# Optimization experiments

Measured on AMD Instinct MI355X. Metric: run time of the kernel, lower is better.

## Reference

```python
import jax, jax.numpy as jnp
import numpy as np

EPS = 1e-5


def _binary_act(x):
    # Forward: sign(x). Backward: piecewise-polynomial surrogate (ApproxSign STE).
    out3 = jnp.where(x < -1, -1.0,
            jnp.where(x < 0, x * x + 2.0 * x,
             jnp.where(x < 1, -x * x + 2.0 * x, 1.0)))
    return jax.lax.stop_gradient(jnp.sign(x) - out3) + out3


def _binarize_weights(w):
    # Per-output-channel scaling factor (detached), forward = scale*sign(w),
    # backward flows through clamp(w, -1, 1) (STE).
    scale = jax.lax.stop_gradient(jnp.mean(jnp.abs(w), axis=(1, 2, 3), keepdims=True))
    clipped = jnp.clip(w, -1.0, 1.0)
    return jax.lax.stop_gradient(scale * jnp.sign(w) - clipped) + clipped


def setup_inputs() -> dict:
    key = jax.random.key(0)
    kx, kw = jax.random.split(key)
    B, Cin, Cout, H, W = 32, 128, 128, 56, 56
    x = jax.random.normal(kx, (B, Cin, H, W), dtype=jnp.float32)
    # HardBinaryConv: weight = rand(n)*0.001 permuted then reshaped -> just random in [0, 0.001)
    w = jax.random.uniform(kw, (Cout, Cin, 3, 3), dtype=jnp.float32) * 0.001
    return {
        "x": x,
        "bias0": jnp.zeros((Cin,), jnp.float32),   # move0 LearnableBias
        "w": w,                                     # HardBinaryConv latent weights
        "gamma": jnp.ones((Cout,), jnp.float32),    # BN weight
        "beta": jnp.zeros((Cout,), jnp.float32),    # BN bias
        "bias1": jnp.zeros((Cout,), jnp.float32),   # move1
        "alpha": jnp.full((Cout,), 0.25, jnp.float32),  # PReLU per-channel
        "bias2": jnp.zeros((Cout,), jnp.float32),   # move2
    }


def reference(x, bias0, w, gamma, beta, bias1, alpha, bias2):
    def pc(v):  # per-channel broadcast (1, C, 1, 1)
        return v[None, :, None, None]

    residual = x
    out = x + pc(bias0)                     # move0
    out = _binary_act(out)                  # binary activation
    bw = _binarize_weights(w)               # {-scale, +scale} weights
    y = jax.lax.conv_general_dilated(
        out, bw, window_strides=(1, 1), padding=((1, 1), (1, 1)),
        dimension_numbers=("NCHW", "OIHW", "NCHW"))
    # BatchNorm2d (training mode: biased batch statistics over N,H,W)
    mean = jnp.mean(y, axis=(0, 2, 3), keepdims=True)
    var = jnp.mean(jnp.square(y - mean), axis=(0, 2, 3), keepdims=True)
    y = (y - mean) * jax.lax.rsqrt(var + EPS) * pc(gamma) + pc(beta)
    y = y + residual
    y = y + pc(bias1)                       # move1
    y = jnp.where(y >= 0, y, pc(alpha) * y)  # PReLU
    y = y + pc(bias2)                       # move2
    return y
```

## Files before the change

### kernel.cpp

```cpp
#include <hip/hip_runtime.h>
#include <stdint.h>

#define NB 32
#define NC 128
#define NH 56
#define NW 56
#define NHW_ (NH * NW)
#define NPIX (NB * NHW_)
#define NO 128
#define NK 1152
#define NSTRIP 14
#define NSLOT (NB * NSTRIP)

#define PADH 58
#define PADW 66
#define PAD_BYTES ((size_t)NB * PADH * PADW * 2 * 8)

typedef unsigned long long u64;

__device__ __forceinline__ size_t pidx(int n, int h, int w) {
    return (((size_t)n * PADH + (h + 1)) * PADW + (w + 1)) * 2;
}

__global__ __launch_bounds__(256) void pack_act(const float* __restrict__ x,
                                                const float* __restrict__ bias0,
                                                u64* __restrict__ packAp) {
    int p = blockIdx.x * 256 + threadIdx.x;
    if (p >= NPIX) return;
    int n = p / NHW_;
    int rem = p - n * NHW_;
    int h = rem / NW, wcol = rem - h * NW;
    const float* xb = x + (size_t)n * NC * NHW_ + rem;
    u64 w0 = 0, w1 = 0;
#pragma unroll 8
    for (int c = 0; c < 64; ++c)
        w0 |= (u64)((xb[(size_t)c * NHW_] + bias0[c]) > 0.f) << c;
#pragma unroll 8
    for (int c = 0; c < 64; ++c)
        w1 |= (u64)((xb[(size_t)(c + 64) * NHW_] + bias0[c + 64]) > 0.f) << c;
    size_t idx = pidx(n, h, wcol);
    packAp[idx]     = w0;
    packAp[idx + 1] = w1;
}

__global__ __launch_bounds__(64) void pack_wgt(const float* __restrict__ w,
                                               u64* __restrict__ packW,
                                               float* __restrict__ scaleW,
                                               int* __restrict__ corrW) {
    __shared__ u64 sb[18];
    int o = blockIdx.x;
    int t = threadIdx.x;
    const float* wo = w + (size_t)o * NK;
    float s = 0.f;
    for (int i = t; i < NK; i += 64) s += fabsf(wo[i]);
    for (int off = 32; off; off >>= 1) s += __shfl_down(s, off);
    if (t == 0) scaleW[o] = s / (float)NK;
    if (t < 18) {
        int tap = t >> 1;
        int j   = t & 1;
        u64 bits = 0;
        for (int cc = 0; cc < 64; ++cc) {
            int c = j * 64 + cc;
            bits |= (u64)(wo[c * 9 + tap] > 0.f) << cc;
        }
        packW[(size_t)o * 18 + t] = bits;
        sb[t] = bits;
    }
    __syncthreads();
    if (t == 0) {
        int cv[9];
#pragma unroll
        for (int tap = 0; tap < 9; ++tap)
            cv[tap] = NC - 2 * (__popcll(sb[2 * tap]) + __popcll(sb[2 * tap + 1]));
        int* cw = corrW + o * 8;
        cw[0] = cv[0] + cv[3] + cv[6];
        cw[1] = cv[2] + cv[5] + cv[8];
        cw[2] = cv[0] + cv[1] + cv[2];
        cw[3] = cv[6] + cv[7] + cv[8];
        cw[4] = cv[0];
        cw[5] = cv[2];
        cw[6] = cv[6];
        cw[7] = cv[8];
    }
}

template <int MODE>
__global__ __launch_bounds__(128, 4) void conv_bin(
    const u64* __restrict__ packAp, const u64* __restrict__ packW,
    const int* __restrict__ corrW, short* __restrict__ yI,
    int* __restrict__ sumP, int* __restrict__ sqP,
    const float* __restrict__ coefA, const float* __restrict__ coefB,
    const float* __restrict__ alpha, const float* __restrict__ bias2,
    const float* __restrict__ x, float* __restrict__ out) {
    __shared__ u64 lw[32 * 18];
    __shared__ int lc[32 * 8];

    int bid = blockIdx.x;
    int n = bid / (NSTRIP * 4);
    int rem = bid - n * (NSTRIP * 4);
    int strip = rem >> 2;
    int cgp = rem & 3;
    int obase = cgp * 32;
    int h0 = strip * 4;

    for (int i = threadIdx.x; i < 32 * 18; i += 128) lw[i] = packW[(size_t)obase * 18 + i];
    for (int i = threadIdx.x; i < 32 * 8; i += 128) lc[i] = corrW[obase * 8 + i];

    int wv = threadIdx.x >> 6, lane = threadIdx.x & 63;
    bool act = lane < NW;

    u64 a[6][3][2];
    const u64* bp = packAp + (((size_t)n * PADH + h0) * PADW + lane) * 2;
#pragma unroll
    for (int r = 0; r < 6; ++r)
#pragma unroll
        for (int c = 0; c < 3; ++c) {
            ulonglong2 q = *reinterpret_cast<const ulonglong2*>(bp + ((size_t)r * PADW + c) * 2);
            a[r][c][0] = q.x;
            a[r][c][1] = q.y;
        }
#pragma unroll
    for (int r = 0; r < 6; ++r)
#pragma unroll
        for (int c = 0; c < 3; ++c)
            asm volatile("" : "+v"(a[r][c][0]), "+v"(a[r][c][1]));
    __syncthreads();

    bool top = (strip == 0), bot = (strip == NSTRIP - 1);
    bool isL = (lane == 0), isR = (lane == NW - 1);
    int sl = n * NSTRIP + strip;
    short* ybase = yI + (size_t)n * NO * NHW_ + (size_t)h0 * NW + lane;

    for (int oo = 0; oo < 16; ++oo) {
        int lo = (wv << 4) + oo;
        int o = obase + lo;
        const u64* wp = &lw[lo * 18];
        int pc0 = 0, pc1 = 0, pc2 = 0, pc3 = 0;
#pragma unroll
        for (int t = 0; t < 9; ++t) {
            const int kh = t / 3, kw = t - 3 * (t / 3);
            u64 w0 = wp[2 * t], w1 = wp[2 * t + 1];
            pc0 += __popcll(a[kh][kw][0] ^ w0) + __popcll(a[kh][kw][1] ^ w1);
            pc1 += __popcll(a[kh + 1][kw][0] ^ w0) + __popcll(a[kh + 1][kw][1] ^ w1);
            pc2 += __popcll(a[kh + 2][kw][0] ^ w0) + __popcll(a[kh + 2][kw][1] ^ w1);
            pc3 += __popcll(a[kh + 3][kw][0] ^ w0) + __popcll(a[kh + 3][kw][1] ^ w1);
        }
        const int* cw = &lc[lo * 8];
        int corrcol = isL ? cw[0] : (isR ? cw[1] : 0);
        int base = NK - corrcol;
        int d0 = base - 2 * pc0;
        int d1 = base - 2 * pc1;
        int d2 = base - 2 * pc2;
        int d3 = base - 2 * pc3;
        if (top) d0 -= cw[2] - (isL ? cw[4] : (isR ? cw[5] : 0));
        if (bot) d3 -= cw[3] - (isL ? cw[6] : (isR ? cw[7] : 0));

        if (MODE == 0 && act) {
            short* yp = ybase + (size_t)o * NHW_;
            yp[0]      = (short)d0;
            yp[NW]     = (short)d1;
            yp[2 * NW] = (short)d2;
            yp[3 * NW] = (short)d3;
        }
        if (MODE <= 1) {
            int s = act ? (d0 + d1 + d2 + d3) : 0;
            int q = act ? (__mul24(d0, d0) + __mul24(d1, d1) +
                           __mul24(d2, d2) + __mul24(d3, d3)) : 0;
#pragma unroll
            for (int off = 32; off; off >>= 1) {
                s += __shfl_down(s, off);
                q += __shfl_down(q, off);
            }
            if (lane == 0) {
                sumP[o * NSLOT + sl] = s;
                sqP[o * NSLOT + sl]  = q;
            }
        }
        if (MODE == 2 && act) {
            float ca = coefA[o], cb = coefB[o], al = alpha[o], b2 = bias2[o];
            size_t idx = ((size_t)n * NO + o) * NHW_ + (size_t)h0 * NW + lane;
            int dv[4] = {d0, d1, d2, d3};
#pragma unroll
            for (int r = 0; r < 4; ++r) {
                float tv = fmaf(ca, (float)dv[r], cb) + x[idx + (size_t)r * NW];
                tv = tv >= 0.f ? tv : al * tv;
                out[idx + (size_t)r * NW] = tv + b2;
            }
        }
    }
}

__global__ __launch_bounds__(64) void bn_coef2(const int* __restrict__ sumP,
                                               const int* __restrict__ sqP,
                                               const float* __restrict__ scaleW,
                                               const float* __restrict__ gamma,
                                               const float* __restrict__ beta,
                                               const float* __restrict__ bias1,
                                               float* __restrict__ coefA,
                                               float* __restrict__ coefB) {
    int o = blockIdx.x;
    int t = threadIdx.x;
    long long s = 0, q = 0;
    for (int i = t; i < NSLOT; i += 64) {
        s += sumP[o * NSLOT + i];
        q += sqP[o * NSLOT + i];
    }
#pragma unroll
    for (int off = 32; off; off >>= 1) {
        s += __shfl_down(s, off);
        q += __shfl_down(q, off);
    }
    if (t == 0) {
        double cnt = (double)NPIX;
        double mean = (double)s / cnt;
        double var = (double)q / cnt - mean * mean;
        if (var < 0.0) var = 0.0;
        float sc = scaleW[o];
        float rs = rsqrtf((float)((double)sc * (double)sc * var) + 1e-5f);
        float g = gamma[o];
        coefA[o] = sc * g * rs;
        coefB[o] = beta[o] - (float)((double)sc * mean) * g * rs + bias1[o];
    }
}

__global__ __launch_bounds__(256) void final_store(const short* __restrict__ yI,
                                                   const float* __restrict__ x,
                                                   const float* __restrict__ coefA,
                                                   const float* __restrict__ coefB,
                                                   const float* __restrict__ alpha,
                                                   const float* __restrict__ bias2,
                                                   float* __restrict__ out) {
    const size_t ngroups = (size_t)NB * NO * NHW_ / 8;
    for (size_t g = (size_t)blockIdx.x * blockDim.x + threadIdx.x; g < ngroups;
         g += (size_t)gridDim.x * blockDim.x) {
        size_t i = g * 8;
        int o = (int)((i / NHW_) % NO);
        float a = coefA[o], bb = coefB[o], al = alpha[o], b2 = bias2[o];
        int4 yv = *reinterpret_cast<const int4*>(yI + i);
        float4 x0 = *reinterpret_cast<const float4*>(x + i);
        float4 x1 = *reinterpret_cast<const float4*>(x + i + 4);
        int q[4] = {yv.x, yv.y, yv.z, yv.w};
        float xs[8] = {x0.x, x0.y, x0.z, x0.w, x1.x, x1.y, x1.z, x1.w};
        float r[8];
#pragma unroll
        for (int j = 0; j < 4; ++j) {
            float lo = (float)(short)(q[j] & 0xffff);
            float hi = (float)(q[j] >> 16);
            float t0 = fmaf(a, lo, bb) + xs[2 * j];
            float t1 = fmaf(a, hi, bb) + xs[2 * j + 1];
            t0 = t0 >= 0.f ? t0 : al * t0;
            t1 = t1 >= 0.f ? t1 : al * t1;
            r[2 * j]     = t0 + b2;
            r[2 * j + 1] = t1 + b2;
        }
        float4 o0 = {r[0], r[1], r[2], r[3]};
        float4 o1 = {r[4], r[5], r[6], r[7]};
        *reinterpret_cast<float4*>(out + i)     = o0;
        *reinterpret_cast<float4*>(out + i + 4) = o1;
    }
}

extern "C" void kernel_launch(void* const* d_in, const int* in_sizes, int n_in,
                              void* d_out, int out_size, void* d_ws, size_t ws_size,
                              hipStream_t stream) {
    (void)in_sizes; (void)n_in; (void)out_size;
    const float* x     = (const float*)d_in[0];
    const float* bias0 = (const float*)d_in[1];
    const float* w     = (const float*)d_in[2];
    const float* gamma = (const float*)d_in[3];
    const float* beta  = (const float*)d_in[4];
    const float* bias1 = (const float*)d_in[5];
    const float* alpha = (const float*)d_in[6];
    const float* bias2 = (const float*)d_in[7];
    float* out = (float*)d_out;
    char* ws = (char*)d_ws;

    u64*   packAp = (u64*)ws;
    u64*   packW  = (u64*)(ws + 1959936);
    int*   corrW  = (int*)(ws + 1978368);
    float* scaleW = (float*)(ws + 1982464);
    float* coefA  = (float*)(ws + 1982976);
    float* coefB  = (float*)(ws + 1983488);
    int*   sumP   = (int*)(ws + 1984000);
    int*   sqP    = (int*)(ws + 2213376);
    short* yI     = (short*)(ws + 2442752);
    bool store = ws_size >= (size_t)2442752 + (size_t)NB * NO * NHW_ * 2;

    hipMemsetAsync(packAp, 0, PAD_BYTES, stream);
    pack_act<<<NPIX / 256, 256, 0, stream>>>(x, bias0, packAp);
    pack_wgt<<<NO, 64, 0, stream>>>(w, packW, scaleW, corrW);

    if (store) {
        conv_bin<0><<<NB * NSTRIP * 4, 128, 0, stream>>>(
            packAp, packW, corrW, yI, sumP, sqP,
            nullptr, nullptr, nullptr, nullptr, nullptr, nullptr);
        bn_coef2<<<NO, 64, 0, stream>>>(sumP, sqP, scaleW, gamma, beta, bias1, coefA, coefB);
        final_store<<<2048, 256, 0, stream>>>(yI, x, coefA, coefB, alpha, bias2, out);
    } else {
        conv_bin<1><<<NB * NSTRIP * 4, 128, 0, stream>>>(
            packAp, packW, corrW, nullptr, sumP, sqP,
            nullptr, nullptr, nullptr, nullptr, nullptr, nullptr);
        bn_coef2<<<NO, 64, 0, stream>>>(sumP, sqP, scaleW, gamma, beta, bias1, coefA, coefB);
        conv_bin<2><<<NB * NSTRIP * 4, 128, 0, stream>>>(
            packAp, packW, corrW, nullptr, sumP, sqP,
            coefA, coefB, alpha, bias2, x, out);
    }
}
```

Measured before the change: 109.7 us.

## Retile binary conv to 2-row strips, read weights directly via scalar loads

The binary conv kernel now has each block cover 2 output rows and 64 output channels with 4 waves of 256 threads, where before it covered 4 rows and 32 channels. The shared-memory weight staging and the __syncthreads are removed. Weights and correction terms are read straight from global memory through a wave-uniform (readfirstlane) base, so they can use scalar loads. This cuts register pressure (4x3 activation rows instead of 6x3) and raises parallelism, at the cost of more redundant activation loads per output and twice as many partial-sum slots for the BN reduction.

```diff
diff --git a/kernel.cpp b/kernel.cpp
--- a/kernel.cpp
+++ b/kernel.cpp
@@ -9,18 +9,14 @@
 #define NPIX (NB * NHW_)
 #define NO 128
 #define NK 1152
-#define NSTRIP 14
-#define NSLOT (NB * NSTRIP)
+#define NRP 28
+#define NSLOT (NB * NRP)
 
 #define PADH 58
 #define PADW 66
 #define PAD_BYTES ((size_t)NB * PADH * PADW * 2 * 8)
 
 typedef unsigned long long u64;
-
-__device__ __forceinline__ size_t pidx(int n, int h, int w) {
-    return (((size_t)n * PADH + (h + 1)) * PADW + (w + 1)) * 2;
-}
 
 __global__ __launch_bounds__(256) void pack_act(const float* __restrict__ x,
                                                 const float* __restrict__ bias0,
@@ -38,7 +34,7 @@
 #pragma unroll 8
     for (int c = 0; c < 64; ++c)
         w1 |= (u64)((xb[(size_t)(c + 64) * NHW_] + bias0[c + 64]) > 0.f) << c;
-    size_t idx = pidx(n, h, wcol);
+    size_t idx = (((size_t)n * PADH + (h + 1)) * PADW + (wcol + 1)) * 2;
     packAp[idx]     = w0;
     packAp[idx + 1] = w1;
 }
@@ -85,87 +81,71 @@
 }
 
 template <int MODE>
-__global__ __launch_bounds__(128, 4) void conv_bin(
+__global__ __launch_bounds__(256) void conv_bin(
     const u64* __restrict__ packAp, const u64* __restrict__ packW,
     const int* __restrict__ corrW, short* __restrict__ yI,
     int* __restrict__ sumP, int* __restrict__ sqP,
     const float* __restrict__ coefA, const float* __restrict__ coefB,
     const float* __restrict__ alpha, const float* __restrict__ bias2,
     const float* __restrict__ x, float* __restrict__ out) {
-    __shared__ u64 lw[32 * 18];
-    __shared__ int lc[32 * 8];
-
     int bid = blockIdx.x;
-    int n = bid / (NSTRIP * 4);
-    int rem = bid - n * (NSTRIP * 4);
-    int strip = rem >> 2;
-    int cgp = rem & 3;
-    int obase = cgp * 32;
-    int h0 = strip * 4;
-
-    for (int i = threadIdx.x; i < 32 * 18; i += 128) lw[i] = packW[(size_t)obase * 18 + i];
-    for (int i = threadIdx.x; i < 32 * 8; i += 128) lc[i] = corrW[obase * 8 + i];
+    int n = bid / (NRP * 2);
+    int rem = bid - n * (NRP * 2);
+    int hp = rem >> 1;
+    int cg = rem & 1;
+    int h0 = hp * 2;
 
     int wv = threadIdx.x >> 6, lane = threadIdx.x & 63;
     bool act = lane < NW;
 
-    u64 a[6][3][2];
+    u64 a[4][3][2];
     const u64* bp = packAp + (((size_t)n * PADH + h0) * PADW + lane) * 2;
 #pragma unroll
-    for (int r = 0; r < 6; ++r)
+    for (int r = 0; r < 4; ++r)
 #pragma unroll
         for (int c = 0; c < 3; ++c) {
-            ulonglong2 q = *reinterpret_cast<const ulonglong2*>(bp + ((size_t)r * PADW + c) * 2);
+            ulonglong2 q = *reinterpret_cast<const ulonglong2*>(
+                bp + ((size_t)r * PADW + c) * 2);
             a[r][c][0] = q.x;
             a[r][c][1] = q.y;
         }
-#pragma unroll
-    for (int r = 0; r < 6; ++r)
-#pragma unroll
-        for (int c = 0; c < 3; ++c)
-            asm volatile("" : "+v"(a[r][c][0]), "+v"(a[r][c][1]));
-    __syncthreads();
-
-    bool top = (strip == 0), bot = (strip == NSTRIP - 1);
+
+    int obase = __builtin_amdgcn_readfirstlane(cg * 64 + (wv << 4));
+    const u64* wbase = packW + (size_t)obase * 18;
+    const int* cbase = corrW + obase * 8;
+
+    bool top = (hp == 0), bot = (hp == NRP - 1);
     bool isL = (lane == 0), isR = (lane == NW - 1);
-    int sl = n * NSTRIP + strip;
-    short* ybase = yI + (size_t)n * NO * NHW_ + (size_t)h0 * NW + lane;
+    int sl = n * NRP + hp;
+    size_t pixoff = (size_t)n * NO * NHW_ + (size_t)h0 * NW + lane;
 
     for (int oo = 0; oo < 16; ++oo) {
-        int lo = (wv << 4) + oo;
-        int o = obase + lo;
-        const u64* wp = &lw[lo * 18];
-        int pc0 = 0, pc1 = 0, pc2 = 0, pc3 = 0;
+        int o = obase + oo;
+        const u64* wp = wbase + oo * 18;
+        const int* cw = cbase + oo * 8;
+        int pc0 = 0, pc1 = 0;
 #pragma unroll
         for (int t = 0; t < 9; ++t) {
             const int kh = t / 3, kw = t - 3 * (t / 3);
             u64 w0 = wp[2 * t], w1 = wp[2 * t + 1];
             pc0 += __popcll(a[kh][kw][0] ^ w0) + __popcll(a[kh][kw][1] ^ w1);
             pc1 += __popcll(a[kh + 1][kw][0] ^ w0) + __popcll(a[kh + 1][kw][1] ^ w1);
-            pc2 += __popcll(a[kh + 2][kw][0] ^ w0) + __popcll(a[kh + 2][kw][1] ^ w1);
-            pc3 += __popcll(a[kh + 3][kw][0] ^ w0) + __popcll(a[kh + 3][kw][1] ^ w1);
-        }
-        const int* cw = &lc[lo * 8];
+        }
         int corrcol = isL ? cw[0] : (isR ? cw[1] : 0);
         int base = NK - corrcol;
         int d0 = base - 2 * pc0;
         int d1 = base - 2 * pc1;
-        int d2 = base - 2 * pc2;
-        int d3 = base - 2 * pc3;
         if (top) d0 -= cw[2] - (isL ? cw[4] : (isR ? cw[5] : 0));
-        if (bot) d3 -= cw[3] - (isL ? cw[6] : (isR ? cw[7] : 0));
+        if (bot) d1 -= cw[3] - (isL ? cw[6] : (isR ? cw[7] : 0));
 
         if (MODE == 0 && act) {
-            short* yp = ybase + (size_t)o * NHW_;
-            yp[0]      = (short)d0;
-            yp[NW]     = (short)d1;
-            yp[2 * NW] = (short)d2;
-            yp[3 * NW] = (short)d3;
+            short* yp = yI + pixoff + (size_t)o * NHW_;
+            yp[0]  = (short)d0;
+            yp[NW] = (short)d1;
         }
         if (MODE <= 1) {
-            int s = act ? (d0 + d1 + d2 + d3) : 0;
-            int q = act ? (__mul24(d0, d0) + __mul24(d1, d1) +
-                           __mul24(d2, d2) + __mul24(d3, d3)) : 0;
+            int s = act ? (d0 + d1) : 0;
+            int q = act ? (__mul24(d0, d0) + __mul24(d1, d1)) : 0;
 #pragma unroll
             for (int off = 32; off; off >>= 1) {
                 s += __shfl_down(s, off);
@@ -178,14 +158,13 @@
         }
         if (MODE == 2 && act) {
             float ca = coefA[o], cb = coefB[o], al = alpha[o], b2 = bias2[o];
-            size_t idx = ((size_t)n * NO + o) * NHW_ + (size_t)h0 * NW + lane;
-            int dv[4] = {d0, d1, d2, d3};
-#pragma unroll
-            for (int r = 0; r < 4; ++r) {
-                float tv = fmaf(ca, (float)dv[r], cb) + x[idx + (size_t)r * NW];
-                tv = tv >= 0.f ? tv : al * tv;
-                out[idx + (size_t)r * NW] = tv + b2;
-            }
+            size_t idx = pixoff + (size_t)o * NHW_;
+            float t0 = fmaf(ca, (float)d0, cb) + x[idx];
+            float t1 = fmaf(ca, (float)d1, cb) + x[idx + NW];
+            t0 = t0 >= 0.f ? t0 : al * t0;
+            t1 = t1 >= 0.f ? t1 : al * t1;
+            out[idx]      = t0 + b2;
+            out[idx + NW] = t1 + b2;
         }
     }
 }
@@ -282,26 +261,26 @@
     float* coefA  = (float*)(ws + 1982976);
     float* coefB  = (float*)(ws + 1983488);
     int*   sumP   = (int*)(ws + 1984000);
-    int*   sqP    = (int*)(ws + 2213376);
-    short* yI     = (short*)(ws + 2442752);
-    bool store = ws_size >= (size_t)2442752 + (size_t)NB * NO * NHW_ * 2;
+    int*   sqP    = (int*)(ws + 2442752);
+    short* yI     = (short*)(ws + 2901504);
+    bool store = ws_size >= (size_t)2901504 + (size_t)NB * NO * NHW_ * 2;
 
     hipMemsetAsync(packAp, 0, PAD_BYTES, stream);
     pack_act<<<NPIX / 256, 256, 0, stream>>>(x, bias0, packAp);
     pack_wgt<<<NO, 64, 0, stream>>>(w, packW, scaleW, corrW);
 
     if (store) {
-        conv_bin<0><<<NB * NSTRIP * 4, 128, 0, stream>>>(
+        conv_bin<0><<<NB * NRP * 2, 256, 0, stream>>>(
             packAp, packW, corrW, yI, sumP, sqP,
             nullptr, nullptr, nullptr, nullptr, nullptr, nullptr);
         bn_coef2<<<NO, 64, 0, stream>>>(sumP, sqP, scaleW, gamma, beta, bias1, coefA, coefB);
         final_store<<<2048, 256, 0, stream>>>(yI, x, coefA, coefB, alpha, bias2, out);
     } else {
-        conv_bin<1><<<NB * NSTRIP * 4, 128, 0, stream>>>(
+        conv_bin<1><<<NB * NRP * 2, 256, 0, stream>>>(
             packAp, packW, corrW, nullptr, sumP, sqP,
             nullptr, nullptr, nullptr, nullptr, nullptr, nullptr);
         bn_coef2<<<NO, 64, 0, stream>>>(sumP, sqP, scaleW, gamma, beta, bias1, coefA, coefB);
-        conv_bin<2><<<NB * NSTRIP * 4, 128, 0, stream>>>(
+        conv_bin<2><<<NB * NRP * 2, 256, 0, stream>>>(
             packAp, packW, corrW, nullptr, sumP, sqP,
             coefA, coefB, alpha, bias2, x, out);
     }
```

Result: faster. 100.3 us (-8.6%).
